# Optimization experiments

Measured on AMD Instinct MI355X. Metric: run time of the kernel, lower is better.

Reference implementation:

```python
import jax, jax.numpy as jnp
import numpy as np

B, T, H, N = 2, 1024, 32, 64
HN = H * N              # 2048 hidden size
KVH, KVD = 8, 512       # GQA kv heads / kv width; repeat = HN // KVD = 4
LW, LA, LV, LG, LK = 64, 64, 32, 128, 32   # wavgk_split_list
EPS = 1e-6

def _rms(x, w):
    xf = x.astype(jnp.float32)
    var = jnp.mean(xf * xf, axis=-1, keepdims=True)
    return (w * (xf * jax.lax.rsqrt(var + EPS))).astype(x.dtype)

def _rot_half(x):
    x1, x2 = jnp.split(x, 2, axis=-1)
    return jnp.concatenate([-x2, x1], axis=-1)

def setup_inputs():
    key = jax.random.key(0)
    ks = iter(jax.random.split(key, 32))
    nrm = lambda s, sc=1.0: jax.random.normal(next(ks), s, jnp.float32) * sc
    d = {
        'x_in': nrm((B, T, HN)),
        'v_first': nrm((B, T, KVH, N)),
        'k_first': nrm((B, T, KVH, N)),
        'state': jnp.zeros((B, H, N, N), jnp.float32),
    }
    pos = jnp.arange(T, dtype=jnp.float32)
    inv = 1.0 / (10000.0 ** (jnp.arange(0, N, 2, dtype=jnp.float32) / N))
    ang = pos[:, None] * inv[None, :]
    ang = jnp.concatenate([ang, ang], axis=-1)   # [T, N]
    d['calc_cos'] = jnp.broadcast_to(jnp.cos(ang), (B, T, N))
    d['calc_sin'] = jnp.broadcast_to(jnp.sin(ang), (B, T, N))
    d.update(
        wavgk1=nrm((HN, LW + LA + LV + LG + LK), 0.02),
        w0=jnp.zeros((HN,), jnp.float32), w2=nrm((LW, HN), 0.02),
        a0=jnp.zeros((HN,), jnp.float32), a2=nrm((LA, HN), 0.02),
        v0=jnp.zeros((KVD,), jnp.float32), v2=nrm((LV, KVD), 0.02),
        g2=nrm((LG, HN), 0.02),
        k0=jnp.zeros((KVD,), jnp.float32), k2=nrm((LK, KVD), 0.02),
        r_k=nrm((H, N), 0.1),
        RKV_w=nrm((HN + 2 * KVD, HN), 0.02),
        O_w=nrm((HN, HN), 0.02),
        R_bias=jnp.zeros((HN,), jnp.float32),
        K_bias=jnp.zeros((KVD,), jnp.float32),
        V_bias=jnp.zeros((KVD,), jnp.float32),
        O_bias=jnp.zeros((HN,), jnp.float32),
        ln_r=jnp.ones((N,), jnp.float32),
        ln_k=jnp.ones((N,), jnp.float32),
        ln1=jnp.ones((HN,), jnp.float32),
    )
    return d

def reference(x_in, v_first, k_first, state, calc_cos, calc_sin, wavgk1, w0, w2,
              a0, a2, v0, v2, g2, k0, k2, r_k, RKV_w, O_w, R_bias, K_bias,
              V_bias, O_bias, ln_r, ln_k, ln1):
    rep = HN // KVD
    x = _rms(x_in, ln1)
    rkv = x @ RKV_w.T                                   # dense form of fpx_matmul
    r, k, v = jnp.split(rkv, [HN, HN + KVD], axis=-1)
    xw, xa, xv, xg, xk = jnp.split(x @ wavgk1, [LW, LW + LA, LW + LA + LV, LW + LA + LV + LG], axis=-1)
    r = r + R_bias; k = k + K_bias; v = v + V_bias
    r = _rms(r.reshape(B, T, H, N), ln_r)
    k = _rms(k.reshape(B, T, KVH, N), ln_k)
    cos, sin = calc_cos[:, :, None, :], calc_sin[:, :, None, :]   # unsqueeze_dim=2
    r = r * cos + _rot_half(r) * sin
    k = k * cos + _rot_half(k) * sin
    v = v.reshape(B, T, KVH, N)
    # layer_id > 0 path: gated residual toward layer-0 v/k
    gate_v = jax.nn.sigmoid(xv @ v2 + v0).reshape(B, T, KVH, N)
    v = v + (v_first - v) * gate_v
    gate_k = jax.nn.sigmoid(xk @ k2 + k0).reshape(B, T, KVH, N)
    k = k + (k_first - k) * gate_k
    w = jnp.tanh(xw) @ w2 + w0
    w = -jax.nn.softplus(-w) - 0.5
    # GQA repeat kv heads to H
    k = jnp.broadcast_to(k[:, :, :, None, :], (B, T, KVH, rep, N)).reshape(B, T, HN)
    v = jnp.broadcast_to(v[:, :, :, None, :], (B, T, KVH, rep, N)).reshape(B, T, HN)
    r = r.reshape(B, T, HN)
    a = jax.nn.sigmoid(xa @ a2 + a0)
    g = jax.nn.sigmoid(xg) @ g2
    kh = k.reshape(B, T, H, N)
    kk = (kh / jnp.maximum(jnp.linalg.norm(kh, axis=-1, keepdims=True), 1e-12)).reshape(B, T, HN)
    k = k * (1.0 - w + a)
    aa, bb = -kk, kk * a
    w = -jnp.exp(w.astype(jnp.float32))                 # log-decay (negative)
    # RWKV-7 recurrence: S <- S*diag(exp(w)) + (S a) b^T + v k^T ; o = S r
    hv = lambda t: jnp.moveaxis(t.reshape(B, T, H, N).astype(jnp.float32), 1, 0)
    def step(S, ts):
        r_t, w_t, k_t, v_t, a_t, b_t = ts               # each [B,H,N]
        sa = jnp.einsum('bhvk,bhk->bhv', S, a_t)
        S = S * jnp.exp(w_t)[:, :, None, :] + sa[..., None] * b_t[:, :, None, :] + v_t[..., None] * k_t[:, :, None, :]
        return S, jnp.einsum('bhvk,bhk->bhv', S, r_t)
    _, o = jax.lax.scan(step, state.astype(jnp.float32), (hv(r), hv(w), hv(k), hv(v), hv(aa), hv(bb)))
    xx = jnp.moveaxis(o, 0, 1).reshape(B, T, HN) * float(N) ** -0.5
    r_, k_, v_ = (t.reshape(B, T, H, N) for t in (r, k, v))
    bonus = (jnp.sum(r_ * k_ * r_k, axis=-1, keepdims=True) * v_).reshape(B, T, HN)
    xx = xx.astype(x_in.dtype) + bonus
    return x_in + (xx * g) @ O_w.T + O_bias
```

## Files before the change

### kernel.cpp

```cpp
#include <hip/hip_runtime.h>
#include <hip/hip_bf16.h>

#define B_ 2
#define T_ 1024
#define H_ 32
#define N_ 64
#define HN_ 2048
#define KVH_ 8
#define KVD_ 512
#define MTOK 2048
#define SMN 7168
#define KCAT 320
#define CH 64
#define NCH 16
#define NCHUNK 1024

typedef __bf16 bf16x8 __attribute__((ext_vector_type(8)));
typedef float f32x4 __attribute__((ext_vector_type(4)));
typedef float f32x2 __attribute__((ext_vector_type(2)));

__device__ __forceinline__ float sigmf(float x) { return 1.f / (1.f + expf(-x)); }

__global__ void f2b_kernel(const float* __restrict__ in, __hip_bfloat16* __restrict__ out, int n) {
    int i = blockIdx.x * 256 + threadIdx.x;
    if (i < n) out[i] = __float2bfloat16(in[i]);
}

__global__ void transpose_f2b_kernel(const float* __restrict__ in, __hip_bfloat16* __restrict__ out,
                                     int rows, int cols) {
    long i = (long)blockIdx.x * 256 + threadIdx.x;
    if (i >= (long)rows * cols) return;
    int c = (int)(i / rows), r = (int)(i % rows);
    out[i] = __float2bfloat16(in[(size_t)r * cols + c]);
}

__global__ void build_wcat_kernel(const float* __restrict__ w2, const float* __restrict__ a2,
                                  const float* __restrict__ v2, const float* __restrict__ g2,
                                  const float* __restrict__ k2, __hip_bfloat16* __restrict__ out) {
    long i = (long)blockIdx.x * 256 + threadIdx.x;
    if (i >= (long)SMN * KCAT) return;
    int j = (int)(i / KCAT), k = (int)(i % KCAT);
    float v = 0.f;
    if (j < 2048)      { if (k < 64)             v = w2[(size_t)k * 2048 + j]; }
    else if (j < 4096) { if (k >= 64 && k < 128)  v = a2[(size_t)(k - 64) * 2048 + (j - 2048)]; }
    else if (j < 4608) { if (k >= 128 && k < 160) v = v2[(size_t)(k - 128) * 512 + (j - 4096)]; }
    else if (j < 6656) { if (k >= 160 && k < 288) v = g2[(size_t)(k - 160) * 2048 + (j - 4608)]; }
    else               { if (k >= 288)            v = k2[(size_t)(k - 288) * 512 + (j - 6656)]; }
    out[i] = __float2bfloat16(v);
}

__global__ __launch_bounds__(256) void rmsnorm_kernel(const float* __restrict__ x,
                                                      const float* __restrict__ ln1,
                                                      __hip_bfloat16* __restrict__ out) {
    const int bt = blockIdx.x, tid = threadIdx.x;
    const float* row = x + (size_t)bt * HN_;
    float4 v0 = *(const float4*)(row + tid * 8);
    float4 v1 = *(const float4*)(row + tid * 8 + 4);
    float s = v0.x*v0.x + v0.y*v0.y + v0.z*v0.z + v0.w*v0.w
            + v1.x*v1.x + v1.y*v1.y + v1.z*v1.z + v1.w*v1.w;
    for (int m = 1; m < 64; m <<= 1) s += __shfl_xor(s, m);
    __shared__ float red[4];
    if ((tid & 63) == 0) red[tid >> 6] = s;
    __syncthreads();
    s = red[0] + red[1] + red[2] + red[3];
    float scale = rsqrtf(s * (1.f / HN_) + 1e-6f);
    float vals[8] = {v0.x, v0.y, v0.z, v0.w, v1.x, v1.y, v1.z, v1.w};
    #pragma unroll
    for (int j = 0; j < 8; ++j)
        out[(size_t)bt * HN_ + tid * 8 + j] = __float2bfloat16(vals[j] * scale * ln1[tid * 8 + j]);
}

__global__ void xwmod_kernel(const float* __restrict__ in, __hip_bfloat16* __restrict__ out) {
    long i = (long)blockIdx.x * 256 + threadIdx.x;
    if (i >= (long)MTOK * KCAT) return;
    int c = (int)(i % KCAT);
    float x = in[i];
    if (c < 64) x = tanhf(x);
    else if (c >= 160 && c < 288) x = sigmf(x);
    out[i] = __float2bfloat16(x);
}

__global__ __launch_bounds__(256) void gemm_bt(const __hip_bfloat16* __restrict__ A,
                                               const __hip_bfloat16* __restrict__ B,
                                               float* __restrict__ C, int M, int N, int K,
                                               const float* __restrict__ bias,
                                               const float* __restrict__ addend) {
    __shared__ __align__(16) __hip_bfloat16 As[64][40];
    __shared__ __align__(16) __hip_bfloat16 Bs[64][40];
    const int tid = threadIdx.x;
    const int wave = tid >> 6, lane = tid & 63;
    const int wr = (wave >> 1) * 32, wc = (wave & 1) * 32;
    const int brow = blockIdx.y << 6, bcol = blockIdx.x << 6;
    const int lrow = tid >> 2, lcol = (tid & 3) << 3;
    const int fr = lane & 15, ko = (lane >> 4) << 3;
    f32x4 acc[2][2] = {};
    for (int k0 = 0; k0 < K; k0 += 32) {
        uint4 av = *(const uint4*)(A + (size_t)(brow + lrow) * K + k0 + lcol);
        uint4 bv = *(const uint4*)(B + (size_t)(bcol + lrow) * K + k0 + lcol);
        *(uint4*)(&As[lrow][lcol]) = av;
        *(uint4*)(&Bs[lrow][lcol]) = bv;
        __syncthreads();
        bf16x8 af0 = *(const bf16x8*)(&As[wr + fr][ko]);
        bf16x8 af1 = *(const bf16x8*)(&As[wr + 16 + fr][ko]);
        bf16x8 bf0 = *(const bf16x8*)(&Bs[wc + fr][ko]);
        bf16x8 bf1 = *(const bf16x8*)(&Bs[wc + 16 + fr][ko]);
        acc[0][0] = __builtin_amdgcn_mfma_f32_16x16x32_bf16(af0, bf0, acc[0][0], 0, 0, 0);
        acc[0][1] = __builtin_amdgcn_mfma_f32_16x16x32_bf16(af0, bf1, acc[0][1], 0, 0, 0);
        acc[1][0] = __builtin_amdgcn_mfma_f32_16x16x32_bf16(af1, bf0, acc[1][0], 0, 0, 0);
        acc[1][1] = __builtin_amdgcn_mfma_f32_16x16x32_bf16(af1, bf1, acc[1][1], 0, 0, 0);
        __syncthreads();
    }
    const int cr = (lane >> 4) << 2, cc = lane & 15;
    #pragma unroll
    for (int i = 0; i < 2; ++i)
        #pragma unroll
        for (int j = 0; j < 2; ++j)
            #pragma unroll
            for (int r = 0; r < 4; ++r) {
                int row = brow + wr + i * 16 + cr + r;
                int col = bcol + wc + j * 16 + cc;
                float v = acc[i][j][r];
                if (bias) v += bias[col];
                if (addend) v += addend[(size_t)row * N + col];
                C[(size_t)row * N + col] = v;
            }
}

__global__ __launch_bounds__(256) void gemm_bt128(const __hip_bfloat16* __restrict__ A,
                                                  const __hip_bfloat16* __restrict__ B,
                                                  float* __restrict__ C, int M, int N, int K,
                                                  const float* __restrict__ bias,
                                                  const float* __restrict__ addend) {
    __shared__ __align__(16) __hip_bfloat16 As[128][40];
    __shared__ __align__(16) __hip_bfloat16 Bs[128][40];
    const int tid = threadIdx.x;
    const int wave = tid >> 6, lane = tid & 63;
    const int wr = (wave >> 1) * 64, wc = (wave & 1) * 64;
    const int brow = blockIdx.y << 7, bcol = blockIdx.x << 7;
    const int lrow = tid >> 2, lcol = (tid & 3) << 3;
    const int fr = lane & 15, ko = (lane >> 4) << 3;
    f32x4 acc[4][4] = {};
    const __hip_bfloat16* Ap = A + (size_t)(brow + lrow) * K + lcol;
    const __hip_bfloat16* Bp = B + (size_t)(bcol + lrow) * K + lcol;
    const size_t half = (size_t)64 * K;
    for (int k0 = 0; k0 < K; k0 += 32) {
        uint4 a0 = *(const uint4*)(Ap + k0);
        uint4 a1 = *(const uint4*)(Ap + half + k0);
        uint4 b0 = *(const uint4*)(Bp + k0);
        uint4 b1 = *(const uint4*)(Bp + half + k0);
        *(uint4*)(&As[lrow][lcol]) = a0;
        *(uint4*)(&As[lrow + 64][lcol]) = a1;
        *(uint4*)(&Bs[lrow][lcol]) = b0;
        *(uint4*)(&Bs[lrow + 64][lcol]) = b1;
        __syncthreads();
        bf16x8 af[4], bfr[4];
        #pragma unroll
        for (int i = 0; i < 4; ++i) {
            af[i]  = *(const bf16x8*)(&As[wr + i * 16 + fr][ko]);
            bfr[i] = *(const bf16x8*)(&Bs[wc + i * 16 + fr][ko]);
        }
        #pragma unroll
        for (int i = 0; i < 4; ++i)
            #pragma unroll
            for (int j = 0; j < 4; ++j)
                acc[i][j] = __builtin_amdgcn_mfma_f32_16x16x32_bf16(af[i], bfr[j], acc[i][j], 0, 0, 0);
        __syncthreads();
    }
    const int cr = (lane >> 4) << 2, cc = lane & 15;
    #pragma unroll
    for (int i = 0; i < 4; ++i)
        #pragma unroll
        for (int j = 0; j < 4; ++j) {
            const int row0 = brow + wr + i * 16 + cr;
            const int col = bcol + wc + j * 16 + cc;
            #pragma unroll
            for (int r = 0; r < 4; ++r) {
                float v = acc[i][j][r];
                if (bias) v += bias[col];
                if (addend) v += addend[(size_t)(row0 + r) * N + col];
                C[(size_t)(row0 + r) * N + col] = v;
            }
        }
}

__global__ __launch_bounds__(256) void compose_kernel(
    const float* __restrict__ RKV, const float* __restrict__ SM,
    const float* __restrict__ v_first, const float* __restrict__ k_first,
    const float* __restrict__ cosd, const float* __restrict__ sind,
    const float* __restrict__ R_bias, const float* __restrict__ K_bias,
    const float* __restrict__ V_bias, const float* __restrict__ w0,
    const float* __restrict__ a0, const float* __restrict__ v0b,
    const float* __restrict__ k0b, const float* __restrict__ ln_r,
    const float* __restrict__ ln_k, const float* __restrict__ r_k,
    char* __restrict__ SC, __hip_bfloat16* __restrict__ VB, float* __restrict__ SB) {
    __shared__ __align__(16) float rbuf[HN_];
    __shared__ __align__(16) float kbuf[KVD_];
    __shared__ __align__(16) float vbuf[KVD_];
    __shared__ float knorms[KVH_];
    __shared__ float cosb[64], sinb[64];
    const int bt = blockIdx.x;
    const int b = bt >> 10, t = bt & 1023;
    const int tid = threadIdx.x;
    const float* rkvrow = RKV + (size_t)bt * 3072;
    const float* smrow = SM + (size_t)bt * SMN;

    if (tid < 64) {
        cosb[tid] = cosd[(size_t)bt * 64 + tid];
        sinb[tid] = sind[(size_t)bt * 64 + tid];
    }

    const int h = tid >> 3;
    const int off = (tid & 7) << 3;
    const int n0 = tid << 3;
    float rraw[8];
    {
        float4 x0 = *(const float4*)(rkvrow + n0);
        float4 x1 = *(const float4*)(rkvrow + n0 + 4);
        float4 b0 = *(const float4*)(R_bias + n0);
        float4 b1 = *(const float4*)(R_bias + n0 + 4);
        rraw[0] = x0.x + b0.x; rraw[1] = x0.y + b0.y; rraw[2] = x0.z + b0.z; rraw[3] = x0.w + b0.w;
        rraw[4] = x1.x + b1.x; rraw[5] = x1.y + b1.y; rraw[6] = x1.z + b1.z; rraw[7] = x1.w + b1.w;
    }
    float rss = 0.f;
    #pragma unroll
    for (int j = 0; j < 8; ++j) { rss += rraw[j] * rraw[j]; rbuf[n0 + j] = rraw[j]; }
    rss += __shfl_xor(rss, 1); rss += __shfl_xor(rss, 2); rss += __shfl_xor(rss, 4);
    float rscale = rsqrtf(rss * (1.f / 64.f) + 1e-6f);

    const int kvh = tid >> 5;
    const int ko2 = (tid & 31) << 1;
    const int kidx = kvh * 64 + ko2;
    float kraw0 = rkvrow[2048 + kidx] + K_bias[kidx];
    float kraw1 = rkvrow[2048 + kidx + 1] + K_bias[kidx + 1];
    float kss = kraw0 * kraw0 + kraw1 * kraw1;
    kss += __shfl_xor(kss, 1); kss += __shfl_xor(kss, 2); kss += __shfl_xor(kss, 4);
    kss += __shfl_xor(kss, 8); kss += __shfl_xor(kss, 16);
    float kscale = rsqrtf(kss * (1.f / 64.f) + 1e-6f);
    kbuf[kidx] = kraw0; kbuf[kidx + 1] = kraw1;

    {
        float va = rkvrow[2560 + kidx] + V_bias[kidx];
        float vb2 = rkvrow[2560 + kidx + 1] + V_bias[kidx + 1];
        float gv0 = sigmf(smrow[4096 + kidx] + v0b[kidx]);
        float gv1 = sigmf(smrow[4096 + kidx + 1] + v0b[kidx + 1]);
        vbuf[kidx] = va + (v_first[(size_t)bt * 512 + kidx] - va) * gv0;
        vbuf[kidx + 1] = vb2 + (v_first[(size_t)bt * 512 + kidx + 1] - vb2) * gv1;
    }
    __syncthreads();

    float rf[8];
    #pragma unroll
    for (int j = 0; j < 8; ++j) {
        int nn = off + j;
        int nn2 = (nn + 32) & 63;
        float val = rbuf[h * 64 + nn] * rscale * ln_r[nn];
        float oth = rbuf[h * 64 + nn2] * rscale * ln_r[nn2];
        float rot = (nn < 32) ? -oth : oth;
        rf[j] = val * cosb[nn] + rot * sinb[nn];
    }
    float kfv[2];
    #pragma unroll
    for (int j = 0; j < 2; ++j) {
        int nn = ko2 + j;
        int nn2 = (nn + 32) & 63;
        float val = kbuf[kvh * 64 + nn] * kscale * ln_k[nn];
        float oth = kbuf[kvh * 64 + nn2] * kscale * ln_k[nn2];
        float rot = (nn < 32) ? -oth : oth;
        float kr = val * cosb[nn] + rot * sinb[nn];
        float gk = sigmf(smrow[6656 + kvh * 64 + nn] + k0b[kvh * 64 + nn]);
        kfv[j] = kr + (k_first[(size_t)bt * 512 + kvh * 64 + nn] - kr) * gk;
    }
    __syncthreads();
    kbuf[kidx] = kfv[0]; kbuf[kidx + 1] = kfv[1];
    float kn = kfv[0] * kfv[0] + kfv[1] * kfv[1];
    kn += __shfl_xor(kn, 1); kn += __shfl_xor(kn, 2); kn += __shfl_xor(kn, 4);
    kn += __shfl_xor(kn, 8); kn += __shfl_xor(kn, 16);
    if ((tid & 31) == 0) knorms[kvh] = fmaxf(sqrtf(kn), 1e-12f);
    __syncthreads();

    const float knv = knorms[h >> 2];
    char* scb = SC + ((size_t)(b * H_ + h) * T_ + t) * 896;
    __hip_bfloat16* us = (__hip_bfloat16*)scb;
    float* df = (float*)(scb + 640);
    float4 w1a = *(const float4*)(smrow + n0);
    float4 w1b = *(const float4*)(smrow + n0 + 4);
    float4 ara = *(const float4*)(smrow + 2048 + n0);
    float4 arb = *(const float4*)(smrow + 2048 + n0 + 4);
    float w1arr[8] = {w1a.x, w1a.y, w1a.z, w1a.w, w1b.x, w1b.y, w1b.z, w1b.w};
    float aarr[8] = {ara.x, ara.y, ara.z, ara.w, arb.x, arb.y, arb.z, arb.w};
    float bsum = 0.f;
    #pragma unroll
    for (int j = 0; j < 8; ++j) {
        int nn = off + j, n = n0 + j;
        float w1 = w1arr[j] + w0[n];
        float w2v = -log1pf(expf(-w1)) - 0.5f;
        float av = sigmf(aarr[j] + a0[n]);
        float dec = expf(-expf(w2v));
        float kb = kbuf[(h >> 2) * 64 + nn];
        float vbv = vbuf[(h >> 2) * 64 + nn];
        float kkv = kb / knv;
        float ksc = kb * (1.f - w2v + av);
        us[nn]       = __float2bfloat16(rf[j]);
        us[64 + nn]  = __float2bfloat16(ksc);
        us[128 + nn] = __float2bfloat16(-kkv);
        us[192 + nn] = __float2bfloat16(kkv * av);
        us[256 + nn] = __float2bfloat16(vbv);
        df[nn] = dec;
        VB[(size_t)bt * HN_ + n] = __float2bfloat16(vbv);
        bsum += rf[j] * ksc * r_k[h * 64 + nn];
    }
    bsum += __shfl_xor(bsum, 1); bsum += __shfl_xor(bsum, 2); bsum += __shfl_xor(bsum, 4);
    if ((tid & 7) == 0) SB[bt * H_ + h] = bsum;
}

__global__ __launch_bounds__(128) void scan_pass1(
    const char* __restrict__ SC, float* __restrict__ Q, float* __restrict__ O,
    float* __restrict__ Pf, float* __restrict__ Sf) {
    const int chunk = blockIdx.x;
    const int bh = chunk >> 4, c = chunk & 15;
    const int b = bh >> 5, h = bh & 31;
    const int tid = threadIdx.x;
    const int wid = tid >> 6, lane = tid & 63;
    const char* base = SC + ((size_t)bh * T_ + (size_t)c * CH) * 896;
    __shared__ __align__(16) float ld[2][5][64];

    f32x4 R4[16];
    #pragma unroll
    for (int j = 0; j < 16; ++j)
        #pragma unroll
        for (int e = 0; e < 4; ++e)
            R4[j][e] = (wid == 0 && 4 * j + e == lane) ? 1.f : 0.f;

    float p0, p1, p2;
    auto LOADT = [&](int t) {
        const __hip_bfloat16* us = (const __hip_bfloat16*)(base + (size_t)t * 896);
        if (wid == 0) {
            p0 = __bfloat162float(us[128 + lane]);
            p1 = __bfloat162float(us[192 + lane]);
            p2 = __bfloat162float(us[lane]);
        } else {
            p0 = *(const float*)(base + (size_t)t * 896 + 640 + 4 * lane);
            p1 = __bfloat162float(us[64 + lane]);
            p2 = __bfloat162float(us[256 + lane]);
        }
    };
    LOADT(0);
    float* qbase = Q + (size_t)chunk * CH * 64 + lane;
    float* obase = O + ((size_t)b * T_ + (size_t)c * CH) * HN_ + h * 64 + lane;
    for (int t = 0; t < CH; ++t) {
        const int buf = t & 1;
        float vt = 0.f;
        if (wid == 0) {
            ld[buf][0][lane] = p0;
            ld[buf][1][lane] = p1;
            ld[buf][4][lane] = p2;
        } else {
            ld[buf][2][lane] = p0;
            ld[buf][3][lane] = p1;
            vt = p2;
        }
        __syncthreads();
        if (t + 1 < CH) LOADT(t + 1);
        f32x4 da = {0,0,0,0}, db = {0,0,0,0};
        #pragma unroll
        for (int j = 0; j < 16; j += 2) {
            da += R4[j]     * *(const f32x4*)&ld[buf][0][4 * j];
            db += R4[j + 1] * *(const f32x4*)&ld[buf][0][4 * j + 4];
        }
        const float dot = da[0] + da[1] + da[2] + da[3] + db[0] + db[1] + db[2] + db[3];
        const f32x4 dotv = {dot, dot, dot, dot};
        f32x4 qa = {0,0,0,0}, qb = {0,0,0,0};
        if (wid == 0) {
            #pragma unroll
            for (int j = 0; j < 16; j += 2) {
                f32x4 d0 = *(const f32x4*)&ld[buf][2][4 * j];
                f32x4 b0 = *(const f32x4*)&ld[buf][1][4 * j];
                f32x4 r0 = *(const f32x4*)&ld[buf][4][4 * j];
                f32x4 Pn = R4[j] * d0 + dotv * b0;
                R4[j] = Pn; qa += Pn * r0;
                f32x4 d1 = *(const f32x4*)&ld[buf][2][4 * j + 4];
                f32x4 b1 = *(const f32x4*)&ld[buf][1][4 * j + 4];
                f32x4 r1 = *(const f32x4*)&ld[buf][4][4 * j + 4];
                f32x4 Pm = R4[j + 1] * d1 + dotv * b1;
                R4[j + 1] = Pm; qb += Pm * r1;
            }
            qbase[(size_t)t * 64] = qa[0]+qa[1]+qa[2]+qa[3]+qb[0]+qb[1]+qb[2]+qb[3];
        } else {
            const f32x4 vtv = {vt, vt, vt, vt};
            #pragma unroll
            for (int j = 0; j < 16; j += 2) {
                f32x4 d0 = *(const f32x4*)&ld[buf][2][4 * j];
                f32x4 b0 = *(const f32x4*)&ld[buf][1][4 * j];
                f32x4 k0 = *(const f32x4*)&ld[buf][3][4 * j];
                f32x4 r0 = *(const f32x4*)&ld[buf][4][4 * j];
                f32x4 Sn = R4[j] * d0 + dotv * b0 + vtv * k0;
                R4[j] = Sn; qa += Sn * r0;
                f32x4 d1 = *(const f32x4*)&ld[buf][2][4 * j + 4];
                f32x4 b1 = *(const f32x4*)&ld[buf][1][4 * j + 4];
                f32x4 k1 = *(const f32x4*)&ld[buf][3][4 * j + 4];
                f32x4 r1 = *(const f32x4*)&ld[buf][4][4 * j + 4];
                f32x4 Sm = R4[j + 1] * d1 + dotv * b1 + vtv * k1;
                R4[j + 1] = Sm; qb += Sm * r1;
            }
            obase[(size_t)t * HN_] = qa[0]+qa[1]+qa[2]+qa[3]+qb[0]+qb[1]+qb[2]+qb[3];
        }
    }
    float* fp = (wid == 0 ? Pf : Sf) + (size_t)chunk * 4096 + lane * 64;
    #pragma unroll
    for (int j = 0; j < 16; ++j)
        *(f32x4*)(fp + 4 * j) = R4[j];
}

__global__ __launch_bounds__(256) void scan_pass2(
    const float* __restrict__ Pf, float* __restrict__ Sf, const float* __restrict__ state) {
    const int blk = blockIdx.x;
    const int bh = blk >> 2, rb = blk & 3;
    const int tid = threadIdx.x;
    const int lv = tid >> 4, c0 = (tid & 15) << 2;
    __shared__ __align__(16) float S[16][68];
    __shared__ __align__(16) float P[64][64];

    *(f32x4*)&S[lv][c0] = *(const f32x4*)&state[(size_t)bh * 4096 + 1024 * rb + tid * 4];
    const size_t pbase = (size_t)(bh * NCH) * 4096;
    {
        f32x4 p0[4];
        #pragma unroll
        for (int j = 0; j < 4; ++j) p0[j] = *(const f32x4*)&Pf[pbase + tid * 16 + 4 * j];
        #pragma unroll
        for (int j = 0; j < 4; ++j) *(f32x4*)(&P[0][0] + tid * 16 + 4 * j) = p0[j];
    }
    __syncthreads();

    for (int c = 0; c < NCH; ++c) {
        const size_t ck = (size_t)(bh * NCH + c) * 4096;
        f32x4 pp[4];
        if (c + 1 < NCH) {
            #pragma unroll
            for (int j = 0; j < 4; ++j) pp[j] = *(const f32x4*)&Pf[ck + 4096 + tid * 16 + 4 * j];
        }
        f32x4 acc = *(const f32x4*)&Sf[ck + 1024 * rb + tid * 4];
        f32x4 cur = *(const f32x4*)&S[lv][c0];
        #pragma unroll 4
        for (int k4 = 0; k4 < 64; k4 += 4) {
            f32x4 sk4 = *(const f32x4*)&S[lv][k4];
            #pragma unroll
            for (int kk = 0; kk < 4; ++kk) {
                f32x4 pr = *(const f32x4*)&P[k4 + kk][c0];
                f32x4 sv = {sk4[kk], sk4[kk], sk4[kk], sk4[kk]};
                acc += sv * pr;
            }
        }
        __syncthreads();
        *(f32x4*)&S[lv][c0] = acc;
        if (c + 1 < NCH) {
            #pragma unroll
            for (int j = 0; j < 4; ++j) *(f32x4*)(&P[0][0] + tid * 16 + 4 * j) = pp[j];
        }
        *(f32x4*)&Sf[ck + 1024 * rb + tid * 4] = cur;
        __syncthreads();
    }
}

__global__ __launch_bounds__(64) void scan_pass3(
    const float* __restrict__ Q, const float* __restrict__ Sinit, float* __restrict__ O) {
    const int chunk = blockIdx.x;
    const int bh = chunk >> 4, c = chunk & 15;
    const int b = bh >> 5, h = bh & 31;
    const int t = threadIdx.x;
    __shared__ __align__(16) float S[64][64];
    #pragma unroll
    for (int j = 0; j < 16; ++j)
        *(f32x4*)&S[t][4 * j] = *(const f32x4*)&Sinit[(size_t)chunk * 4096 + (size_t)t * 64 + 4 * j];
    __syncthreads();
    float q[64];
    #pragma unroll
    for (int j = 0; j < 16; ++j)
        *(f32x4*)&q[4 * j] = *(const f32x4*)&Q[((size_t)chunk * CH + t) * 64 + 4 * j];
    float* orow = O + ((size_t)b * T_ + (size_t)c * CH + t) * HN_ + h * 64;
    #pragma unroll 4
    for (int v = 0; v < 64; ++v) {
        f32x4 a = {0, 0, 0, 0};
        #pragma unroll
        for (int j = 0; j < 16; ++j)
            a += *(const f32x4*)&S[v][4 * j] * *(const f32x4*)&q[4 * j];
        orow[v] = (a[0] + a[1] + a[2] + a[3] + orow[v]) * 0.125f;
    }
}

__global__ void post_kernel(const float* __restrict__ O, const float* __restrict__ SB,
                            const __hip_bfloat16* __restrict__ VB, const float* __restrict__ SM,
                            __hip_bfloat16* __restrict__ Ub) {
    long i = (long)blockIdx.x * 256 + threadIdx.x;
    if (i >= (long)MTOK * HN_) return;
    int bt = (int)(i >> 11), n = (int)(i & 2047), h = n >> 6;
    float u = (O[i] + SB[bt * H_ + h] * __bfloat162float(VB[i])) * SM[(size_t)bt * SMN + 4608 + n];
    Ub[i] = __float2bfloat16(u);
}

extern "C" void kernel_launch(void* const* d_in, const int* in_sizes, int n_in,
                              void* d_out, int out_size, void* d_ws, size_t ws_size,
                              hipStream_t stream) {
    (void)in_sizes; (void)n_in; (void)out_size; (void)ws_size;
    const float* x_in    = (const float*)d_in[0];
    const float* v_first = (const float*)d_in[1];
    const float* k_first = (const float*)d_in[2];
    const float* state   = (const float*)d_in[3];
    const float* calc_cos= (const float*)d_in[4];
    const float* calc_sin= (const float*)d_in[5];
    const float* wavgk1  = (const float*)d_in[6];
    const float* w0      = (const float*)d_in[7];
    const float* w2      = (const float*)d_in[8];
    const float* a0      = (const float*)d_in[9];
    const float* a2      = (const float*)d_in[10];
    const float* v0      = (const float*)d_in[11];
    const float* v2      = (const float*)d_in[12];
    const float* g2      = (const float*)d_in[13];
    const float* k0      = (const float*)d_in[14];
    const float* k2      = (const float*)d_in[15];
    const float* r_k     = (const float*)d_in[16];
    const float* RKV_w   = (const float*)d_in[17];
    const float* O_w     = (const float*)d_in[18];
    const float* R_bias  = (const float*)d_in[19];
    const float* K_bias  = (const float*)d_in[20];
    const float* V_bias  = (const float*)d_in[21];
    const float* O_bias  = (const float*)d_in[22];
    const float* ln_r    = (const float*)d_in[23];
    const float* ln_k    = (const float*)d_in[24];
    const float* ln1     = (const float*)d_in[25];
    float* out = (float*)d_out;

    char* ws = (char*)d_ws;
    size_t off = 0;
    auto alloc = [&](size_t bytes) -> char* {
        char* p = ws + off;
        off = (off + bytes + 255) & ~(size_t)255;
        return p;
    };
    float* SMf = (float*)alloc((size_t)MTOK * SMN * 4);
    char*  SCb = alloc((size_t)64 * T_ * 896);
    __hip_bfloat16* Ub = (__hip_bfloat16*)SCb;
    __hip_bfloat16* VBb = (__hip_bfloat16*)alloc((size_t)MTOK * HN_ * 2);
    float* SBf = (float*)alloc((size_t)MTOK * H_ * 4);
    float* Of  = (float*)alloc((size_t)MTOK * HN_ * 4);
    __hip_bfloat16* OWb = (__hip_bfloat16*)alloc((size_t)2048 * 2048 * 2);

    size_t ovl = off;
    __hip_bfloat16* Xb     = (__hip_bfloat16*)alloc((size_t)MTOK * HN_ * 2);
    __hip_bfloat16* RKVb   = (__hip_bfloat16*)alloc((size_t)3072 * 2048 * 2);
    __hip_bfloat16* WT1b   = (__hip_bfloat16*)alloc((size_t)320 * 2048 * 2);
    __hip_bfloat16* Wcatb  = (__hip_bfloat16*)alloc((size_t)SMN * KCAT * 2);
    __hip_bfloat16* XWmodb = (__hip_bfloat16*)alloc((size_t)MTOK * KCAT * 2);
    float* RKVf  = (float*)alloc((size_t)MTOK * 3072 * 4);
    float* XWraw = (float*)alloc((size_t)MTOK * KCAT * 4);
    off = ovl;
    float* Qf  = (float*)alloc((size_t)NCHUNK * CH * 64 * 4);
    float* Pff = (float*)alloc((size_t)NCHUNK * 4096 * 4);
    float* Sff = (float*)alloc((size_t)NCHUNK * 4096 * 4);

    f2b_kernel<<<(3072 * 2048 + 255) / 256, 256, 0, stream>>>(RKV_w, RKVb, 3072 * 2048);
    f2b_kernel<<<(2048 * 2048 + 255) / 256, 256, 0, stream>>>(O_w, OWb, 2048 * 2048);
    transpose_f2b_kernel<<<(320 * 2048 + 255) / 256, 256, 0, stream>>>(wavgk1, WT1b, 2048, 320);
    build_wcat_kernel<<<(SMN * KCAT + 255) / 256, 256, 0, stream>>>(w2, a2, v2, g2, k2, Wcatb);

    rmsnorm_kernel<<<MTOK, 256, 0, stream>>>(x_in, ln1, Xb);

    gemm_bt128<<<dim3(3072 / 128, MTOK / 128), 256, 0, stream>>>(Xb, RKVb, RKVf, MTOK, 3072, 2048, nullptr, nullptr);
    gemm_bt<<<dim3(320 / 64, MTOK / 64), 256, 0, stream>>>(Xb, WT1b, XWraw, MTOK, 320, 2048, nullptr, nullptr);
    xwmod_kernel<<<(MTOK * KCAT + 255) / 256, 256, 0, stream>>>(XWraw, XWmodb);
    gemm_bt128<<<dim3(SMN / 128, MTOK / 128), 256, 0, stream>>>(XWmodb, Wcatb, SMf, MTOK, SMN, KCAT, nullptr, nullptr);

    compose_kernel<<<MTOK, 256, 0, stream>>>(RKVf, SMf, v_first, k_first, calc_cos, calc_sin,
                                             R_bias, K_bias, V_bias, w0, a0, v0, k0,
                                             ln_r, ln_k, r_k, SCb, VBb, SBf);

    scan_pass1<<<NCHUNK, 128, 0, stream>>>(SCb, Qf, Of, Pff, Sff);
    scan_pass2<<<B_ * H_ * 4, 256, 0, stream>>>(Pff, Sff, state);
    scan_pass3<<<NCHUNK, 64, 0, stream>>>(Qf, Sff, Of);

    post_kernel<<<(MTOK * HN_ + 255) / 256, 256, 0, stream>>>(Of, SBf, VBb, SMf, Ub);
    gemm_bt128<<<dim3(HN_ / 128, MTOK / 128), 256, 0, stream>>>(Ub, OWb, out, MTOK, HN_, 2048, O_bias, x_in);
}
```

Measured before the change: 462.4 us.

## Split scan_pass1 rows across two lanes to double threads per chunk

The chunked scan's first pass now uses 256 threads per block instead of 128. Each P/S state row is split into two 32-column halves held by lanes 32 apart, and partial dot products are combined with a cross-half shuffle. This halves per-thread register state and serial FMA work per timestep, which raises occupancy and shortens the latency-bound recurrence. In exchange it adds extra shuffles per step and changes how the loads are spread across four waves.

```diff
diff --git a/kernel.cpp b/kernel.cpp
--- a/kernel.cpp
+++ b/kernel.cpp
@@ -313,7 +313,7 @@
     if ((tid & 7) == 0) SB[bt * H_ + h] = bsum;
 }
 
-__global__ __launch_bounds__(128) void scan_pass1(
+__global__ __launch_bounds__(256) void scan_pass1(
     const char* __restrict__ SC, float* __restrict__ Q, float* __restrict__ O,
     float* __restrict__ Pf, float* __restrict__ Sf) {
     const int chunk = blockIdx.x;
@@ -321,93 +321,95 @@
     const int b = bh >> 5, h = bh & 31;
     const int tid = threadIdx.x;
     const int wid = tid >> 6, lane = tid & 63;
+    const int mat = wid >> 1;
+    const int rhalf = wid & 1;
+    const int row = rhalf * 32 + (lane & 31);
+    const int chalf = lane >> 5;
+    const int cb = chalf * 32;
     const char* base = SC + ((size_t)bh * T_ + (size_t)c * CH) * 896;
     __shared__ __align__(16) float ld[2][5][64];
 
-    f32x4 R4[16];
-    #pragma unroll
-    for (int j = 0; j < 16; ++j)
+    f32x4 R4[8];
+    #pragma unroll
+    for (int j = 0; j < 8; ++j)
         #pragma unroll
         for (int e = 0; e < 4; ++e)
-            R4[j][e] = (wid == 0 && 4 * j + e == lane) ? 1.f : 0.f;
-
-    float p0, p1, p2;
+            R4[j][e] = (mat == 0 && cb + 4 * j + e == row) ? 1.f : 0.f;
+
+    float p0, p1;
     auto LOADT = [&](int t) {
         const __hip_bfloat16* us = (const __hip_bfloat16*)(base + (size_t)t * 896);
-        if (wid == 0) {
-            p0 = __bfloat162float(us[128 + lane]);
-            p1 = __bfloat162float(us[192 + lane]);
-            p2 = __bfloat162float(us[lane]);
-        } else {
-            p0 = *(const float*)(base + (size_t)t * 896 + 640 + 4 * lane);
-            p1 = __bfloat162float(us[64 + lane]);
-            p2 = __bfloat162float(us[256 + lane]);
-        }
+        if (wid == 0)      { p0 = __bfloat162float(us[128 + lane]); p1 = __bfloat162float(us[lane]); }
+        else if (wid == 1) { p0 = __bfloat162float(us[192 + lane]); p1 = 0.f; }
+        else if (wid == 2) { p0 = *(const float*)(base + (size_t)t * 896 + 640 + 4 * lane);
+                             p1 = __bfloat162float(us[256 + (lane & 31)]); }
+        else               { p0 = __bfloat162float(us[64 + lane]);
+                             p1 = __bfloat162float(us[256 + 32 + (lane & 31)]); }
     };
     LOADT(0);
-    float* qbase = Q + (size_t)chunk * CH * 64 + lane;
-    float* obase = O + ((size_t)b * T_ + (size_t)c * CH) * HN_ + h * 64 + lane;
+    float* qrow = Q + (size_t)chunk * CH * 64 + row;
+    float* orow = O + ((size_t)b * T_ + (size_t)c * CH) * HN_ + h * 64 + row;
     for (int t = 0; t < CH; ++t) {
         const int buf = t & 1;
-        float vt = 0.f;
-        if (wid == 0) {
-            ld[buf][0][lane] = p0;
-            ld[buf][1][lane] = p1;
-            ld[buf][4][lane] = p2;
-        } else {
-            ld[buf][2][lane] = p0;
-            ld[buf][3][lane] = p1;
-            vt = p2;
-        }
+        float vt = p1;
+        if (wid == 0)      { ld[buf][0][lane] = p0; ld[buf][4][lane] = p1; }
+        else if (wid == 1) { ld[buf][1][lane] = p0; }
+        else if (wid == 2) { ld[buf][2][lane] = p0; }
+        else               { ld[buf][3][lane] = p0; }
         __syncthreads();
         if (t + 1 < CH) LOADT(t + 1);
         f32x4 da = {0,0,0,0}, db = {0,0,0,0};
         #pragma unroll
-        for (int j = 0; j < 16; j += 2) {
-            da += R4[j]     * *(const f32x4*)&ld[buf][0][4 * j];
-            db += R4[j + 1] * *(const f32x4*)&ld[buf][0][4 * j + 4];
-        }
-        const float dot = da[0] + da[1] + da[2] + da[3] + db[0] + db[1] + db[2] + db[3];
+        for (int j = 0; j < 8; j += 2) {
+            da += R4[j]     * *(const f32x4*)&ld[buf][0][cb + 4 * j];
+            db += R4[j + 1] * *(const f32x4*)&ld[buf][0][cb + 4 * j + 4];
+        }
+        float dot = da[0] + da[1] + da[2] + da[3] + db[0] + db[1] + db[2] + db[3];
+        dot += __shfl_xor(dot, 32);
         const f32x4 dotv = {dot, dot, dot, dot};
         f32x4 qa = {0,0,0,0}, qb = {0,0,0,0};
-        if (wid == 0) {
-            #pragma unroll
-            for (int j = 0; j < 16; j += 2) {
-                f32x4 d0 = *(const f32x4*)&ld[buf][2][4 * j];
-                f32x4 b0 = *(const f32x4*)&ld[buf][1][4 * j];
-                f32x4 r0 = *(const f32x4*)&ld[buf][4][4 * j];
+        if (mat == 0) {
+            #pragma unroll
+            for (int j = 0; j < 8; j += 2) {
+                f32x4 d0 = *(const f32x4*)&ld[buf][2][cb + 4 * j];
+                f32x4 b0 = *(const f32x4*)&ld[buf][1][cb + 4 * j];
+                f32x4 r0 = *(const f32x4*)&ld[buf][4][cb + 4 * j];
                 f32x4 Pn = R4[j] * d0 + dotv * b0;
                 R4[j] = Pn; qa += Pn * r0;
-                f32x4 d1 = *(const f32x4*)&ld[buf][2][4 * j + 4];
-                f32x4 b1 = *(const f32x4*)&ld[buf][1][4 * j + 4];
-                f32x4 r1 = *(const f32x4*)&ld[buf][4][4 * j + 4];
+                f32x4 d1 = *(const f32x4*)&ld[buf][2][cb + 4 * j + 4];
+                f32x4 b1 = *(const f32x4*)&ld[buf][1][cb + 4 * j + 4];
+                f32x4 r1 = *(const f32x4*)&ld[buf][4][cb + 4 * j + 4];
                 f32x4 Pm = R4[j + 1] * d1 + dotv * b1;
                 R4[j + 1] = Pm; qb += Pm * r1;
             }
-            qbase[(size_t)t * 64] = qa[0]+qa[1]+qa[2]+qa[3]+qb[0]+qb[1]+qb[2]+qb[3];
+            float qs = qa[0]+qa[1]+qa[2]+qa[3]+qb[0]+qb[1]+qb[2]+qb[3];
+            qs += __shfl_xor(qs, 32);
+            if (chalf == 0) qrow[(size_t)t * 64] = qs;
         } else {
             const f32x4 vtv = {vt, vt, vt, vt};
             #pragma unroll
-            for (int j = 0; j < 16; j += 2) {
-                f32x4 d0 = *(const f32x4*)&ld[buf][2][4 * j];
-                f32x4 b0 = *(const f32x4*)&ld[buf][1][4 * j];
-                f32x4 k0 = *(const f32x4*)&ld[buf][3][4 * j];
-                f32x4 r0 = *(const f32x4*)&ld[buf][4][4 * j];
+            for (int j = 0; j < 8; j += 2) {
+                f32x4 d0 = *(const f32x4*)&ld[buf][2][cb + 4 * j];
+                f32x4 b0 = *(const f32x4*)&ld[buf][1][cb + 4 * j];
+                f32x4 k0 = *(const f32x4*)&ld[buf][3][cb + 4 * j];
+                f32x4 r0 = *(const f32x4*)&ld[buf][4][cb + 4 * j];
                 f32x4 Sn = R4[j] * d0 + dotv * b0 + vtv * k0;
                 R4[j] = Sn; qa += Sn * r0;
-                f32x4 d1 = *(const f32x4*)&ld[buf][2][4 * j + 4];
-                f32x4 b1 = *(const f32x4*)&ld[buf][1][4 * j + 4];
-                f32x4 k1 = *(const f32x4*)&ld[buf][3][4 * j + 4];
-                f32x4 r1 = *(const f32x4*)&ld[buf][4][4 * j + 4];
+                f32x4 d1 = *(const f32x4*)&ld[buf][2][cb + 4 * j + 4];
+                f32x4 b1 = *(const f32x4*)&ld[buf][1][cb + 4 * j + 4];
+                f32x4 k1 = *(const f32x4*)&ld[buf][3][cb + 4 * j + 4];
+                f32x4 r1 = *(const f32x4*)&ld[buf][4][cb + 4 * j + 4];
                 f32x4 Sm = R4[j + 1] * d1 + dotv * b1 + vtv * k1;
                 R4[j + 1] = Sm; qb += Sm * r1;
             }
-            obase[(size_t)t * HN_] = qa[0]+qa[1]+qa[2]+qa[3]+qb[0]+qb[1]+qb[2]+qb[3];
-        }
-    }
-    float* fp = (wid == 0 ? Pf : Sf) + (size_t)chunk * 4096 + lane * 64;
-    #pragma unroll
-    for (int j = 0; j < 16; ++j)
+            float os = qa[0]+qa[1]+qa[2]+qa[3]+qb[0]+qb[1]+qb[2]+qb[3];
+            os += __shfl_xor(os, 32);
+            if (chalf == 0) orow[(size_t)t * HN_] = os;
+        }
+    }
+    float* fp = (mat == 0 ? Pf : Sf) + (size_t)chunk * 4096 + (size_t)row * 64 + cb;
+    #pragma unroll
+    for (int j = 0; j < 8; ++j)
         *(f32x4*)(fp + 4 * j) = R4[j];
 }
 
@@ -573,7 +575,7 @@
                                              R_bias, K_bias, V_bias, w0, a0, v0, k0,
                                              ln_r, ln_k, r_k, SCb, VBb, SBf);
 
-    scan_pass1<<<NCHUNK, 128, 0, stream>>>(SCb, Qf, Of, Pff, Sff);
+    scan_pass1<<<NCHUNK, 256, 0, stream>>>(SCb, Qf, Of, Pff, Sff);
     scan_pass2<<<B_ * H_ * 4, 256, 0, stream>>>(Pff, Sff, state);
     scan_pass3<<<NCHUNK, 64, 0, stream>>>(Qf, Sff, Of);
 
```

After: 459.0 us. Within noise of the previous version (-0.7%).
